# Performance work log

Measured on AMD Instinct MI355X. Metric: run time of the kernel, lower is better.

Reference implementation:

```python
import jax, jax.numpy as jnp
import numpy as np

B = 16384
D = 4096  # d_mlp == d_hidden in this module
K = 64


def setup_inputs() -> dict:
    key = jax.random.key(0)
    k1, k2, k3, k4 = jax.random.split(key, 4)
    x = jax.random.normal(k1, (B, D), dtype=jnp.float32)
    ema_frequency_counter = jax.random.uniform(k2, (D,), dtype=jnp.float32)
    W_enc = jax.random.normal(k3, (D, D), dtype=jnp.float32)
    # W_dec initialized like the module: randn, then scaled by 0.1/(norm+2*eps-ish);
    # the exact init scaling: norm over dim=1, norm += eps(=1), then *= 0.1/(norm+eps)
    W_dec_raw = jax.random.normal(k4, (D, D), dtype=jnp.float32)
    eps = 1.0
    norm = jnp.linalg.norm(W_dec_raw, axis=1, keepdims=True) + eps
    W_dec = W_dec_raw * (0.1 / (norm + eps))
    pre_bias = jnp.zeros((D,), dtype=jnp.float32)
    latent_bias = jnp.zeros((D,), dtype=jnp.float32)
    return {
        'x': x,
        'ema_frequency_counter': ema_frequency_counter,
        'W_enc': W_enc,
        'W_dec': W_dec,
        'pre_bias': pre_bias,
        'latent_bias': latent_bias,
        'k': K,
    }


def topk_activation(acts, k):
    # torch.topk -> ReLU on values -> scatter back into zeros
    vals, idx = jax.lax.top_k(acts, k)          # [B, k]
    vals = jax.nn.relu(vals)
    rows = jnp.arange(acts.shape[0])[:, None]   # [B, 1]
    return jnp.zeros_like(acts).at[rows, idx].set(vals)


def reference(x, ema_frequency_counter, W_enc, W_dec, pre_bias, latent_bias, k):
    # method='reconstruct' path of TopKAutoEncoder.forward
    x_center = x - pre_bias                     # [B, D]
    acts = x_center @ W_enc + latent_bias       # [B, D]
    acts_top_k = topk_activation(acts, k)       # sparse (k nonzeros/row)
    x_reconstruct = acts_top_k @ W_dec + pre_bias
    return x_reconstruct
```

## Files before the change

### kernel.cpp

```cpp
#include <hip/hip_runtime.h>
#include <hip/hip_bf16.h>
#include <stdint.h>


typedef _Float16 half8 __attribute__((ext_vector_type(8)));
typedef float f32x4 __attribute__((ext_vector_type(4)));
typedef unsigned short ushort8 __attribute__((ext_vector_type(8)));

#define B_ROWS 16384
#define D_DIM  4096
#define TOPK   64
#define MARGIN 0.25f
#define NTILES (D_DIM / 32)

__device__ __forceinline__ void gload_lds16(const void* g, void* l) {
  __builtin_amdgcn_global_load_lds(
      (const __attribute__((address_space(1))) unsigned int*)g,
      (__attribute__((address_space(3))) unsigned int*)l, 16, 0, 0);
}

__device__ __forceinline__ unsigned f32_sortable(float f) {
  unsigned u = __float_as_uint(f);
  return (u & 0x80000000u) ? ~u : (u | 0x80000000u);
}
__device__ __forceinline__ float sortable_f32(unsigned u) {
  return __uint_as_float((u & 0x80000000u) ? (u & 0x7fffffffu) : ~u);
}
__device__ __forceinline__ unsigned short f2bf(float f) {
  unsigned u = __float_as_uint(f);
  unsigned r = (u + 0x7fffu + ((u >> 16) & 1u)) >> 16;
  return (unsigned short)r;
}


__global__ __launch_bounds__(256) void conv_x(
    const float* __restrict__ x, const float* __restrict__ pre_bias,
    _Float16* __restrict__ Xh) {
  size_t g = ((size_t)blockIdx.x * 256 + threadIdx.x) * 8;
  int col = (int)(g & (D_DIM - 1));
  float4 a = *(const float4*)(x + g);
  float4 b = *(const float4*)(x + g + 4);
  float4 p = *(const float4*)(pre_bias + col);
  float4 q = *(const float4*)(pre_bias + col + 4);
  half8 h;
  h[0] = (_Float16)(a.x - p.x); h[1] = (_Float16)(a.y - p.y);
  h[2] = (_Float16)(a.z - p.z); h[3] = (_Float16)(a.w - p.w);
  h[4] = (_Float16)(b.x - q.x); h[5] = (_Float16)(b.y - q.y);
  h[6] = (_Float16)(b.z - q.z); h[7] = (_Float16)(b.w - q.w);
  *(half8*)(Xh + g) = h;
}

__global__ __launch_bounds__(256) void transp_w(
    const float* __restrict__ W, _Float16* __restrict__ WhT,
    float* __restrict__ WT) {
  __shared__ float tile[64][65];
  int bx = blockIdx.x, by = blockIdx.y;
  int tx = threadIdx.x & 63, ty4 = threadIdx.x >> 6;
  #pragma unroll 4
  for (int i = 0; i < 16; ++i) {
    int r = ty4 * 16 + i;
    tile[r][tx] = W[(size_t)(by * 64 + r) * D_DIM + bx * 64 + tx];
  }
  __syncthreads();
  #pragma unroll 4
  for (int i = 0; i < 16; ++i) {
    int r = ty4 * 16 + i;
    float v = tile[tx][r];
    size_t o = (size_t)(bx * 64 + r) * D_DIM + by * 64 + tx;
    WT[o] = v;
    WhT[o] = (_Float16)v;
  }
}

__global__ __launch_bounds__(256) void conv_wd(
    const float* __restrict__ W, unsigned short* __restrict__ o) {
  size_t g = ((size_t)blockIdx.x * 256 + threadIdx.x) * 8;
  float4 a = *(const float4*)(W + g);
  float4 b = *(const float4*)(W + g + 4);
  ushort8 v;
  v[0] = f2bf(a.x); v[1] = f2bf(a.y); v[2] = f2bf(a.z); v[3] = f2bf(a.w);
  v[4] = f2bf(b.x); v[5] = f2bf(b.y); v[6] = f2bf(b.z); v[7] = f2bf(b.w);
  *(ushort8*)(o + g) = v;
}


#define STAGE(T)                                                               \
  do {                                                                         \
    const int bo_ = ((T) & 3) * 8192;                                          \
    const int kk_ = (T) * 32;                                                  \
    gload_lds16(aSrc0 + kk_, AsB + bo_ + dst0);                                \
    gload_lds16(aSrc1 + kk_, AsB + bo_ + dst1);                                \
    gload_lds16(bSrc0 + kk_, BsB + bo_ + dst0);                                \
    gload_lds16(bSrc1 + kk_, BsB + bo_ + dst1);                                \
  } while (0)

#define PREFETCH(T, AF, BF)                                                    \
  do {                                                                         \
    const int ab_ = ((T) & 3) * 8192;                                          \
    _Pragma("unroll") for (int nj = 0; nj < 4; ++nj)                           \
        BF[nj] = *(const half8*)(BsB + ab_ + bBase + nj * 512);                \
    _Pragma("unroll") for (int mi = 0; mi < 4; ++mi)                           \
        AF[mi] = *(const half8*)(AsB + ab_ + aBase + mi * 512);                \
  } while (0)

#define BODY(T, AFC, BFC, AFN, BFN, VMSTR)                                     \
  do {                                                                         \
    asm volatile("s_waitcnt " VMSTR ::: "memory");                             \
    __builtin_amdgcn_s_barrier();                                              \
    asm volatile("" ::: "memory");                                             \
    if ((T) + 3 < NTILES) STAGE((T) + 3);                                      \
    if ((T) + 1 < NTILES) PREFETCH((T) + 1, AFN, BFN);                         \
    __builtin_amdgcn_s_setprio(1);                                             \
    _Pragma("unroll") for (int mi = 0; mi < 4; ++mi)                           \
        _Pragma("unroll") for (int nj = 0; nj < 4; ++nj)                       \
        acc[mi][nj] = __builtin_amdgcn_mfma_f32_16x16x32_f16(                  \
            AFC[mi], BFC[nj], acc[mi][nj], 0, 0, 0);                           \
    __builtin_amdgcn_s_setprio(0);                                             \
    {                                                                          \
      const int ab_ = ((T) & 3) * 8192;                                        \
      half8 af2[4];                                                            \
      _Pragma("unroll") for (int mi = 0; mi < 4; ++mi)                         \
          af2[mi] = *(const half8*)(AsB + ab_ + aBase + (mi + 4) * 512);       \
      __builtin_amdgcn_s_setprio(1);                                           \
      _Pragma("unroll") for (int mi = 0; mi < 4; ++mi)                         \
          _Pragma("unroll") for (int nj = 0; nj < 4; ++nj)                     \
          acc[mi + 4][nj] = __builtin_amdgcn_mfma_f32_16x16x32_f16(            \
              af2[mi], BFC[nj], acc[mi + 4][nj], 0, 0, 0);                     \
      __builtin_amdgcn_s_setprio(0);                                           \
    }                                                                          \
  } while (0)

__global__ __launch_bounds__(512, 2) void gemm_f16(
    const _Float16* __restrict__ A, const _Float16* __restrict__ Bt,
    const float* __restrict__ latent_bias, float* __restrict__ C) {
  extern __shared__ _Float16 ldsbuf[];
  _Float16* AsB = ldsbuf;
  _Float16* BsB = ldsbuf + 4 * 8192;

  const int tid = threadIdx.x;
  const int lane = tid & 63, wave = tid >> 6;
  const int wr = wave >> 2, wc = wave & 3;

  int bid = blockIdx.x;
  int swz = (bid & 7) * (1024 >> 3) + (bid >> 3);
  const int bmBase = (swz >> 4) * 256;
  const int bnBase = (swz & 15) * 256;

  const int i0 = tid, i1 = 512 + tid;
  const int s0 = i0 ^ ((i0 >> 3) & 3), s1 = i1 ^ ((i1 >> 3) & 3);
  const _Float16* aSrc0 = A + (size_t)(bmBase + (s0 >> 2)) * D_DIM + (s0 & 3) * 8;
  const _Float16* aSrc1 = A + (size_t)(bmBase + (s1 >> 2)) * D_DIM + (s1 & 3) * 8;
  const _Float16* bSrc0 = Bt + (size_t)(bnBase + (s0 >> 2)) * D_DIM + (s0 & 3) * 8;
  const _Float16* bSrc1 = Bt + (size_t)(bnBase + (s1 >> 2)) * D_DIM + (s1 & 3) * 8;
  const int dst0 = i0 * 8, dst1 = i1 * 8;

  const int fr = lane & 15, c4 = lane >> 4;
  const int swzc = (c4 ^ ((fr >> 1) & 3)) * 8;
  const int aBase = (wr * 128 + fr) * 32 + swzc;
  const int bBase = (wc * 64 + fr) * 32 + swzc;

  f32x4 acc[8][4];
  #pragma unroll
  for (int i = 0; i < 8; ++i)
    #pragma unroll
    for (int j = 0; j < 4; ++j) acc[i][j] = f32x4{0.f, 0.f, 0.f, 0.f};

  STAGE(0); STAGE(1); STAGE(2);
  asm volatile("s_waitcnt vmcnt(8)" ::: "memory");
  __builtin_amdgcn_s_barrier();
  asm volatile("" ::: "memory");
  half8 afA[4], bfA[4], afB[4], bfB[4];
  PREFETCH(0, afA, bfA);

  for (int t = 0; t < NTILES - 2; t += 2) {
    BODY(t, afA, bfA, afB, bfB, "vmcnt(4)");
    BODY(t + 1, afB, bfB, afA, bfA, "vmcnt(4)");
  }
  BODY(NTILES - 2, afA, bfA, afB, bfB, "vmcnt(0)");
  BODY(NTILES - 1, afB, bfB, afA, bfA, "vmcnt(0)");

  const int crow0 = bmBase + wr * 128 + c4 * 4;
  const int ccol0 = bnBase + wc * 64 + fr;
  #pragma unroll
  for (int mi = 0; mi < 8; ++mi)
    #pragma unroll
    for (int nj = 0; nj < 4; ++nj) {
      int col = ccol0 + nj * 16;
      float lb = latent_bias[col];
      #pragma unroll
      for (int r = 0; r < 4; ++r)
        C[(size_t)(crow0 + mi * 16 + r) * D_DIM + col] = acc[mi][nj][r] + lb;
    }
}


__global__ __launch_bounds__(256) void topk_classify(
    const float* __restrict__ acts, float* __restrict__ vals,
    int* __restrict__ idxs, int* __restrict__ ambIdx,
    int* __restrict__ rowMeta) {
  const int row = blockIdx.x;
  const int tid = threadIdx.x;
  const int lane = tid & 63, wave = tid >> 6;
  __shared__ int sred[4];
  const float* arow = acts + (size_t)row * D_DIM;
  unsigned su[16];
  #pragma unroll
  for (int i = 0; i < 4; ++i) {
    float4 a = *(const float4*)(arow + i * 1024 + tid * 4);
    su[4 * i + 0] = f32_sortable(a.x);
    su[4 * i + 1] = f32_sortable(a.y);
    su[4 * i + 2] = f32_sortable(a.z);
    su[4 * i + 3] = f32_sortable(a.w);
  }
  unsigned thr = 0u;
  for (int b = 31; b >= 12; --b) {
    unsigned cand = thr | (1u << b);
    int c = 0;
    #pragma unroll
    for (int i = 0; i < 16; ++i) c += (su[i] >= cand) ? 1 : 0;
    #pragma unroll
    for (int off = 32; off; off >>= 1) c += __shfl_down(c, off);
    if (lane == 0) sred[wave] = c;
    __syncthreads();
    int tot = sred[0] + sred[1] + sred[2] + sred[3];
    if (tot >= TOPK) thr = cand;
    __syncthreads();
  }
  float Tlo = sortable_f32(thr);
  float Thi = sortable_f32(thr + 4096u);
  unsigned uhi = f32_sortable(Thi + MARGIN);
  unsigned ulo = f32_sortable(Tlo - MARGIN);
  int mC = 0, aC = 0;
  #pragma unroll
  for (int i = 0; i < 16; ++i) {
    unsigned u = su[i];
    if (u > uhi) ++mC;
    else if (u >= ulo) ++aC;
  }
  int xs = mC | (aC << 16);
  #pragma unroll
  for (int off = 1; off < 64; off <<= 1) {
    int y = __shfl_up(xs, off);
    if (lane >= off) xs += y;
  }
  if (lane == 63) sred[wave] = xs;
  __syncthreads();
  int base = 0;
  for (int w = 0; w < 4; ++w)
    if (w < wave) base += sred[w];
  int tot = sred[0] + sred[1] + sred[2] + sred[3];
  int incl = base + xs;
  int mp = (incl & 0xffff) - mC;
  int ap = (incl >> 16) - aC;
  int mTot = tot & 0xffff, aTot = tot >> 16;
  const int need = TOPK - mTot;
  const bool fast = (aTot == need);
  #pragma unroll
  for (int e = 0; e < 16; ++e) {
    unsigned u = su[e];
    int d = (e >> 2) * 1024 + tid * 4 + (e & 3);
    if (u > uhi) {
      vals[(size_t)row * TOPK + mp] = fmaxf(sortable_f32(u), 0.0f);
      idxs[(size_t)row * TOPK + mp] = d;
      ++mp;
    } else if (u >= ulo) {
      if (fast) {
        vals[(size_t)row * TOPK + mTot + ap] = fmaxf(sortable_f32(u), 0.0f);
        idxs[(size_t)row * TOPK + mTot + ap] = d;
      } else if (ap < 128) {
        ambIdx[(size_t)row * 128 + ap] = d;
      }
      ++ap;
    }
  }
  if (tid == 0) {
    rowMeta[row * 2 + 0] = mTot;
    rowMeta[row * 2 + 1] = (fast || need <= 0) ? 0 : ((aTot > 128) ? 128 : aTot);
  }
}


__global__ __launch_bounds__(256) void rescue(
    const float* __restrict__ x, const float* __restrict__ WT,
    const float* __restrict__ pre_bias, const float* __restrict__ latent_bias,
    const float* __restrict__ acts, const int* __restrict__ ambIdx,
    const int* __restrict__ rowMeta, float* __restrict__ vals,
    int* __restrict__ idxs) {
  const int row = blockIdx.x;
  const int m = rowMeta[row * 2 + 0];
  const int s = rowMeta[row * 2 + 1];
  const int need = TOPK - m;
  const int tid = threadIdx.x;
  if (need <= 0 || s <= 0) return;
  if (s == need) {
    if (tid < s) {
      int d = ambIdx[(size_t)row * 128 + tid];
      float v = acts[(size_t)row * D_DIM + d];
      vals[(size_t)row * TOPK + m + tid] = fmaxf(v, 0.0f);
      idxs[(size_t)row * TOPK + m + tid] = d;
    }
    return;
  }
  __shared__ double exv[128];
  const int lane = tid & 63, wave = tid >> 6;
  const float* xr = x + (size_t)row * D_DIM;
  for (int c = wave; c < s; c += 4) {
    int d = ambIdx[(size_t)row * 128 + c];
    const float* wrow = WT + (size_t)d * D_DIM;
    double acc = 0.0;
    #pragma unroll 4
    for (int t = 0; t < 16; ++t) {
      int k0 = t * 256 + lane * 4;
      float4 xv = *(const float4*)(xr + k0);
      float4 pv = *(const float4*)(pre_bias + k0);
      float4 wv = *(const float4*)(wrow + k0);
      acc = fma((double)xv.x - (double)pv.x, (double)wv.x, acc);
      acc = fma((double)xv.y - (double)pv.y, (double)wv.y, acc);
      acc = fma((double)xv.z - (double)pv.z, (double)wv.z, acc);
      acc = fma((double)xv.w - (double)pv.w, (double)wv.w, acc);
    }
    #pragma unroll
    for (int off = 32; off; off >>= 1) acc += __shfl_down(acc, off);
    if (lane == 0) exv[c] = acc + (double)latent_bias[d];
  }
  __syncthreads();
  if (tid == 0) {
    for (int t = 0; t < need; ++t) {
      double best = -1.0e300; int besti = 1 << 30; int bestc = -1;
      for (int c = 0; c < s; ++c) {
        double v = exv[c];
        int d = ambIdx[(size_t)row * 128 + c];
        if (v > best || (v == best && d < besti)) {
          best = v; besti = d; bestc = c;
        }
      }
      vals[(size_t)row * TOPK + m + t] = fmaxf((float)best, 0.0f);
      idxs[(size_t)row * TOPK + m + t] = besti;
      exv[bestc] = -1.0e300;
    }
  }
}


__global__ __launch_bounds__(256) void reconstruct(
    const unsigned short* __restrict__ Wd, const float* __restrict__ vals,
    const int* __restrict__ idxs, const float* __restrict__ pre_bias,
    float* __restrict__ out) {
  const int bid = blockIdx.x;
  const int cb = bid & 7, rowblk = bid >> 3;
  const int tid = threadIdx.x, lane = tid & 63, wave = tid >> 6;
  const int row = rowblk * 4 + wave;
  const int col0 = cb * 512 + lane * 8;
  __shared__ float sval[256];
  __shared__ int sidx[256];
  sval[tid] = vals[(size_t)(rowblk * 4 + (tid >> 6)) * TOPK + (tid & 63)];
  sidx[tid] = idxs[(size_t)(rowblk * 4 + (tid >> 6)) * TOPK + (tid & 63)];
  __syncthreads();
  float acc[8];
  float4 p0 = *(const float4*)(pre_bias + col0);
  float4 p1 = *(const float4*)(pre_bias + col0 + 4);
  acc[0] = p0.x; acc[1] = p0.y; acc[2] = p0.z; acc[3] = p0.w;
  acc[4] = p1.x; acc[5] = p1.y; acc[6] = p1.z; acc[7] = p1.w;
  #pragma unroll 4
  for (int k = 0; k < TOPK; ++k) {
    float v = sval[wave * 64 + k];
    int d = sidx[wave * 64 + k];
    ushort8 w = *(const ushort8*)(Wd + (size_t)d * D_DIM + col0);
    #pragma unroll
    for (int j = 0; j < 8; ++j)
      acc[j] = fmaf(v, __uint_as_float(((unsigned)w[j]) << 16), acc[j]);
  }
  float4 o0 = {acc[0], acc[1], acc[2], acc[3]};
  float4 o1 = {acc[4], acc[5], acc[6], acc[7]};
  *(float4*)(out + (size_t)row * D_DIM + col0) = o0;
  *(float4*)(out + (size_t)row * D_DIM + col0 + 4) = o1;
}


extern "C" void kernel_launch(void* const* d_in, const int* in_sizes, int n_in,
                              void* d_out, int out_size, void* d_ws,
                              size_t ws_size, hipStream_t stream) {
  const float* x           = (const float*)d_in[0];
  const float* W_enc       = (const float*)d_in[2];
  const float* W_dec       = (const float*)d_in[3];
  const float* pre_bias    = (const float*)d_in[4];
  const float* latent_bias = (const float*)d_in[5];
  float* out = (float*)d_out;
  char* ws = (char*)d_ws;
  size_t off = 0;
  auto alloc = [&](size_t bytes) {
    size_t o = off;
    off = (off + bytes + 255) & ~(size_t)255;
    return o;
  };
  _Float16* Xh        = (_Float16*)(ws + alloc((size_t)B_ROWS * D_DIM * 2));
  _Float16* WhT       = (_Float16*)(ws + alloc((size_t)D_DIM * D_DIM * 2));
  float* WT           = (float*)(ws + alloc((size_t)D_DIM * D_DIM * 4));
  unsigned short* Wd  = (unsigned short*)(ws + alloc((size_t)D_DIM * D_DIM * 2));
  float* vals         = (float*)(ws + alloc((size_t)B_ROWS * TOPK * 4));
  int* idxs           = (int*)(ws + alloc((size_t)B_ROWS * TOPK * 4));
  int* ambIdx         = (int*)(ws + alloc((size_t)B_ROWS * 128 * 4));
  int* rowMeta        = (int*)(ws + alloc((size_t)B_ROWS * 2 * 4));
  (void)ws_size; (void)in_sizes; (void)n_in; (void)out_size;

  (void)hipFuncSetAttribute((const void*)gemm_f16,
                            hipFuncAttributeMaxDynamicSharedMemorySize,
                            131072);

  conv_x<<<(B_ROWS * D_DIM / 8) / 256, 256, 0, stream>>>(x, pre_bias, Xh);
  transp_w<<<dim3(D_DIM / 64, D_DIM / 64), 256, 0, stream>>>(W_enc, WhT, WT);
  conv_wd<<<((size_t)D_DIM * D_DIM / 8) / 256, 256, 0, stream>>>(W_dec, Wd);
  gemm_f16<<<(B_ROWS / 256) * (D_DIM / 256), 512, 131072, stream>>>(
      Xh, WhT, latent_bias, out);
  topk_classify<<<B_ROWS, 256, 0, stream>>>(out, vals, idxs, ambIdx, rowMeta);
  rescue<<<B_ROWS, 256, 0, stream>>>(x, WT, pre_bias, latent_bias, out,
                                     ambIdx, rowMeta, vals, idxs);
  reconstruct<<<(B_ROWS / 4) * 8, 256, 0, stream>>>(Wd, vals, idxs, pre_bias,
                                                    out);
}
```

Measured before the change: 1.209 ms.

## Rework encoder GEMM to 256x128 tiles with 32x32x16 MFMA and 3-stage LDS ring

The fp16 encoder GEMM now uses 256x128 block tiles instead of 256x256 and computes with 32x32x16 MFMA instructions. Each wave holds four 32x32 accumulators, where before it held a grid of 16x16 fragments. LDS drops to 72KB in a three-buffer ring so four blocks can share a CU, which aims to raise occupancy and latency hiding. In exchange, data reuse per block is lower and B traffic rises, and the register-level prefetch of fragments across iterations is gone.

```diff
diff --git a/kernel.cpp b/kernel.cpp
--- a/kernel.cpp
+++ b/kernel.cpp
@@ -5,6 +5,7 @@
 
 typedef _Float16 half8 __attribute__((ext_vector_type(8)));
 typedef float f32x4 __attribute__((ext_vector_type(4)));
+typedef float f32x16 __attribute__((ext_vector_type(16)));
 typedef unsigned short ushort8 __attribute__((ext_vector_type(8)));
 
 #define B_ROWS 16384
@@ -84,113 +85,100 @@
 }
 
 
-#define STAGE(T)                                                               \
+#define STAGE3(KK, BS)                                                         \
   do {                                                                         \
-    const int bo_ = ((T) & 3) * 8192;                                          \
-    const int kk_ = (T) * 32;                                                  \
-    gload_lds16(aSrc0 + kk_, AsB + bo_ + dst0);                                \
-    gload_lds16(aSrc1 + kk_, AsB + bo_ + dst1);                                \
-    gload_lds16(bSrc0 + kk_, BsB + bo_ + dst0);                                \
-    gload_lds16(bSrc1 + kk_, BsB + bo_ + dst1);                                \
+    gload_lds16(aSrc0 + (KK), lds + (BS) + dA0);                               \
+    gload_lds16(aSrc1 + (KK), lds + (BS) + dA1);                               \
+    gload_lds16(bSrc + (KK), lds + (BS) + dB);                                 \
   } while (0)
 
-#define PREFETCH(T, AF, BF)                                                    \
+#define GBODY(DOSTAGE, KK, VMSTR)                                              \
   do {                                                                         \
-    const int ab_ = ((T) & 3) * 8192;                                          \
-    _Pragma("unroll") for (int nj = 0; nj < 4; ++nj)                           \
-        BF[nj] = *(const half8*)(BsB + ab_ + bBase + nj * 512);                \
-    _Pragma("unroll") for (int mi = 0; mi < 4; ++mi)                           \
-        AF[mi] = *(const half8*)(AsB + ab_ + aBase + mi * 512);                \
-  } while (0)
-
-#define BODY(T, AFC, BFC, AFN, BFN, VMSTR)                                     \
-  do {                                                                         \
+    if (DOSTAGE) STAGE3((KK), boffS);                                          \
+    _Pragma("unroll") for (int ks = 0; ks < 2; ++ks) {                         \
+      const int kx = ks * 16;                       \
+      half8 a0 = *(const half8*)(lds + boffC + (aOff ^ kx));                   \
+      half8 a1 = *(const half8*)(lds + boffC + (aOff ^ kx) + 1024);            \
+      half8 b0 = *(const half8*)(lds + boffC + (bOff ^ kx));                   \
+      half8 b1 = *(const half8*)(lds + boffC + (bOff ^ kx) + 1024);            \
+      __builtin_amdgcn_s_setprio(1);                                           \
+      acc00 = __builtin_amdgcn_mfma_f32_32x32x16_f16(a0, b0, acc00, 0, 0, 0);  \
+      acc01 = __builtin_amdgcn_mfma_f32_32x32x16_f16(a0, b1, acc01, 0, 0, 0);  \
+      acc10 = __builtin_amdgcn_mfma_f32_32x32x16_f16(a1, b0, acc10, 0, 0, 0);  \
+      acc11 = __builtin_amdgcn_mfma_f32_32x32x16_f16(a1, b1, acc11, 0, 0, 0);  \
+      __builtin_amdgcn_s_setprio(0);                                           \
+    }                                                                          \
     asm volatile("s_waitcnt " VMSTR ::: "memory");                             \
     __builtin_amdgcn_s_barrier();                                              \
     asm volatile("" ::: "memory");                                             \
-    if ((T) + 3 < NTILES) STAGE((T) + 3);                                      \
-    if ((T) + 1 < NTILES) PREFETCH((T) + 1, AFN, BFN);                         \
-    __builtin_amdgcn_s_setprio(1);                                             \
-    _Pragma("unroll") for (int mi = 0; mi < 4; ++mi)                           \
-        _Pragma("unroll") for (int nj = 0; nj < 4; ++nj)                       \
-        acc[mi][nj] = __builtin_amdgcn_mfma_f32_16x16x32_f16(                  \
-            AFC[mi], BFC[nj], acc[mi][nj], 0, 0, 0);                           \
-    __builtin_amdgcn_s_setprio(0);                                             \
-    {                                                                          \
-      const int ab_ = ((T) & 3) * 8192;                                        \
-      half8 af2[4];                                                            \
-      _Pragma("unroll") for (int mi = 0; mi < 4; ++mi)                         \
-          af2[mi] = *(const half8*)(AsB + ab_ + aBase + (mi + 4) * 512);       \
-      __builtin_amdgcn_s_setprio(1);                                           \
-      _Pragma("unroll") for (int mi = 0; mi < 4; ++mi)                         \
-          _Pragma("unroll") for (int nj = 0; nj < 4; ++nj)                     \
-          acc[mi + 4][nj] = __builtin_amdgcn_mfma_f32_16x16x32_f16(            \
-              af2[mi], BFC[nj], acc[mi + 4][nj], 0, 0, 0);                     \
-      __builtin_amdgcn_s_setprio(0);                                           \
-    }                                                                          \
   } while (0)
 
-__global__ __launch_bounds__(512, 2) void gemm_f16(
+#define GROT()                                                                 \
+  do {                                                                         \
+    boffC += 12288; if (boffC == 36864) boffC = 0;                             \
+    boffS += 12288; if (boffS == 36864) boffS = 0;                             \
+  } while (0)
+
+__global__ __launch_bounds__(512, 4) void gemm_f16(
     const _Float16* __restrict__ A, const _Float16* __restrict__ Bt,
     const float* __restrict__ latent_bias, float* __restrict__ C) {
-  extern __shared__ _Float16 ldsbuf[];
-  _Float16* AsB = ldsbuf;
-  _Float16* BsB = ldsbuf + 4 * 8192;
-
+  extern __shared__ _Float16 lds[];
   const int tid = threadIdx.x;
-  const int lane = tid & 63, wave = tid >> 6;
-  const int wr = wave >> 2, wc = wave & 3;
+  const int lane = tid & 63, l31 = lane & 31, lhi = lane >> 5;
+  const int wave = tid >> 6, wvm = wave & 3, wvn = wave >> 2;
 
   int bid = blockIdx.x;
-  int swz = (bid & 7) * (1024 >> 3) + (bid >> 3);
-  const int bmBase = (swz >> 4) * 256;
-  const int bnBase = (swz & 15) * 256;
-
-  const int i0 = tid, i1 = 512 + tid;
-  const int s0 = i0 ^ ((i0 >> 3) & 3), s1 = i1 ^ ((i1 >> 3) & 3);
-  const _Float16* aSrc0 = A + (size_t)(bmBase + (s0 >> 2)) * D_DIM + (s0 & 3) * 8;
-  const _Float16* aSrc1 = A + (size_t)(bmBase + (s1 >> 2)) * D_DIM + (s1 & 3) * 8;
-  const _Float16* bSrc0 = Bt + (size_t)(bnBase + (s0 >> 2)) * D_DIM + (s0 & 3) * 8;
-  const _Float16* bSrc1 = Bt + (size_t)(bnBase + (s1 >> 2)) * D_DIM + (s1 & 3) * 8;
-  const int dst0 = i0 * 8, dst1 = i1 * 8;
-
-  const int fr = lane & 15, c4 = lane >> 4;
-  const int swzc = (c4 ^ ((fr >> 1) & 3)) * 8;
-  const int aBase = (wr * 128 + fr) * 32 + swzc;
-  const int bBase = (wc * 64 + fr) * 32 + swzc;
-
-  f32x4 acc[8][4];
-  #pragma unroll
-  for (int i = 0; i < 8; ++i)
-    #pragma unroll
-    for (int j = 0; j < 4; ++j) acc[i][j] = f32x4{0.f, 0.f, 0.f, 0.f};
-
-  STAGE(0); STAGE(1); STAGE(2);
-  asm volatile("s_waitcnt vmcnt(8)" ::: "memory");
+  int swz = (bid & 7) * (2048 >> 3) + (bid >> 3);
+  const int bmBase = (swz >> 5) * 256;
+  const int bnBase = (swz & 31) * 128;
+
+  const int pA0 = tid, pA1 = 512 + tid, pB = tid;
+  const int sA0 = pA0 ^ ((pA0 >> 3) & 3), sA1 = pA1 ^ ((pA1 >> 3) & 3);
+  const int sB = pB ^ ((pB >> 3) & 3);
+  const _Float16* aSrc0 = A + (size_t)(bmBase + (sA0 >> 2)) * D_DIM + (sA0 & 3) * 8;
+  const _Float16* aSrc1 = A + (size_t)(bmBase + (sA1 >> 2)) * D_DIM + (sA1 & 3) * 8;
+  const _Float16* bSrc  = Bt + (size_t)(bnBase + (sB >> 2)) * D_DIM + (sB & 3) * 8;
+  const int dA0 = pA0 * 8, dA1 = pA1 * 8, dB = 8192 + pB * 8;
+
+  const int cp0 = lhi ^ ((l31 >> 1) & 3);
+  const int aOff = (wvm * 64 + l31) * 32 + cp0 * 8;
+  const int bOff = 8192 + (wvn * 64 + l31) * 32 + cp0 * 8;
+
+  f32x16 acc00, acc01, acc10, acc11;
+  #pragma unroll
+  for (int i = 0; i < 16; ++i) {
+    acc00[i] = 0.f; acc01[i] = 0.f; acc10[i] = 0.f; acc11[i] = 0.f;
+  }
+
+  int boffC = 0, boffS = 24576;
+  STAGE3(0, 0);
+  STAGE3(32, 12288);
+  asm volatile("s_waitcnt vmcnt(3)" ::: "memory");
   __builtin_amdgcn_s_barrier();
   asm volatile("" ::: "memory");
-  half8 afA[4], bfA[4], afB[4], bfB[4];
-  PREFETCH(0, afA, bfA);
-
-  for (int t = 0; t < NTILES - 2; t += 2) {
-    BODY(t, afA, bfA, afB, bfB, "vmcnt(4)");
-    BODY(t + 1, afB, bfB, afA, bfA, "vmcnt(4)");
-  }
-  BODY(NTILES - 2, afA, bfA, afB, bfB, "vmcnt(0)");
-  BODY(NTILES - 1, afB, bfB, afA, bfA, "vmcnt(0)");
-
-  const int crow0 = bmBase + wr * 128 + c4 * 4;
-  const int ccol0 = bnBase + wc * 64 + fr;
-  #pragma unroll
-  for (int mi = 0; mi < 8; ++mi)
-    #pragma unroll
-    for (int nj = 0; nj < 4; ++nj) {
-      int col = ccol0 + nj * 16;
-      float lb = latent_bias[col];
-      #pragma unroll
-      for (int r = 0; r < 4; ++r)
-        C[(size_t)(crow0 + mi * 16 + r) * D_DIM + col] = acc[mi][nj][r] + lb;
-    }
+
+  for (int t = 0; t < NTILES - 3; ++t) {
+    GBODY(true, (t + 2) * 32, "vmcnt(3)");
+    GROT();
+  }
+  GBODY(true, (NTILES - 1) * 32, "vmcnt(0)");
+  GROT();
+  GBODY(false, 0, "vmcnt(0)");
+  GROT();
+  GBODY(false, 0, "vmcnt(0)");
+
+  const int crow0 = bmBase + wvm * 64;
+  const int ccol0 = bnBase + wvn * 64;
+  const float lb0 = latent_bias[ccol0 + l31];
+  const float lb1 = latent_bias[ccol0 + 32 + l31];
+  #pragma unroll
+  for (int r = 0; r < 16; ++r) {
+    const int rr = (r & 3) + 8 * (r >> 2) + 4 * lhi;
+    C[(size_t)(crow0 + rr) * D_DIM + ccol0 + l31] = acc00[r] + lb0;
+    C[(size_t)(crow0 + rr) * D_DIM + ccol0 + 32 + l31] = acc01[r] + lb1;
+    C[(size_t)(crow0 + 32 + rr) * D_DIM + ccol0 + l31] = acc10[r] + lb0;
+    C[(size_t)(crow0 + 32 + rr) * D_DIM + ccol0 + 32 + l31] = acc11[r] + lb1;
+  }
 }
 
 
@@ -405,12 +393,12 @@
 
   (void)hipFuncSetAttribute((const void*)gemm_f16,
                             hipFuncAttributeMaxDynamicSharedMemorySize,
-                            131072);
+                            73728);
 
   conv_x<<<(B_ROWS * D_DIM / 8) / 256, 256, 0, stream>>>(x, pre_bias, Xh);
   transp_w<<<dim3(D_DIM / 64, D_DIM / 64), 256, 0, stream>>>(W_enc, WhT, WT);
   conv_wd<<<((size_t)D_DIM * D_DIM / 8) / 256, 256, 0, stream>>>(W_dec, Wd);
-  gemm_f16<<<(B_ROWS / 256) * (D_DIM / 256), 512, 131072, stream>>>(
+  gemm_f16<<<(B_ROWS / 256) * (D_DIM / 128), 512, 73728, stream>>>(
       Xh, WhT, latent_bias, out);
   topk_classify<<<B_ROWS, 256, 0, stream>>>(out, vals, idxs, ambIdx, rowMeta);
   rescue<<<B_ROWS, 256, 0, stream>>>(x, WT, pre_bias, latent_bias, out,
```

New measurement: 1.321 ms. 9.3% more time.

## Restructure GEMM main loop into 8-wave ping-pong phases with 64-wide K tiles

Applied to the files above, without the earlier changes.

Replaces the 4-stage, 32-wide-K circular LDS pipeline with a double-buffered 64-wide-K scheme. Each K tile is split into four phases, each doing an LDS fragment read, one async global-to-LDS stage of A or B for the next tile, a barrier, and 16 MFMAs. The goal is to interleave memory staging with MFMA work more finely, in an hipBLASLt-style ping-pong schedule. It adds more barriers per tile and less prefetch depth, which could stall waves if global latency is not covered.

```diff
diff --git a/kernel.cpp b/kernel.cpp
--- a/kernel.cpp
+++ b/kernel.cpp
@@ -11,7 +11,7 @@
 #define D_DIM  4096
 #define TOPK   64
 #define MARGIN 0.25f
-#define NTILES (D_DIM / 32)
+#define KTILES (D_DIM / 64)
 
 __device__ __forceinline__ void gload_lds16(const void* g, void* l) {
   __builtin_amdgcn_global_load_lds(
@@ -84,59 +84,54 @@
 }
 
 
-#define STAGE(T)                                                               \
+#define STG_A(T, KH)                                                           \
   do {                                                                         \
-    const int bo_ = ((T) & 3) * 8192;                                          \
-    const int kk_ = (T) * 32;                                                  \
-    gload_lds16(aSrc0 + kk_, AsB + bo_ + dst0);                                \
-    gload_lds16(aSrc1 + kk_, AsB + bo_ + dst1);                                \
-    gload_lds16(bSrc0 + kk_, BsB + bo_ + dst0);                                \
-    gload_lds16(bSrc1 + kk_, BsB + bo_ + dst1);                                \
+    const int ds_ = ((T) & 1) * 32768 + (KH) * 8192;                           \
+    const int ko_ = (T) * 64 + (KH) * 32;                                      \
+    gload_lds16(aS0 + ko_, lds + ds_ + i0 * 8);                                \
+    gload_lds16(aS1 + ko_, lds + ds_ + i1 * 8);                                \
   } while (0)
 
-#define PREFETCH(T, AF, BF)                                                    \
+#define STG_B(T, KH)                                                           \
   do {                                                                         \
-    const int ab_ = ((T) & 3) * 8192;                                          \
-    _Pragma("unroll") for (int nj = 0; nj < 4; ++nj)                           \
-        BF[nj] = *(const half8*)(BsB + ab_ + bBase + nj * 512);                \
-    _Pragma("unroll") for (int mi = 0; mi < 4; ++mi)                           \
-        AF[mi] = *(const half8*)(AsB + ab_ + aBase + mi * 512);                \
+    const int ds_ = ((T) & 1) * 32768 + 16384 + (KH) * 8192;                   \
+    const int ko_ = (T) * 64 + (KH) * 32;                                      \
+    gload_lds16(bS0 + ko_, lds + ds_ + i0 * 8);                                \
+    gload_lds16(bS1 + ko_, lds + ds_ + i1 * 8);                                \
   } while (0)
 
-#define BODY(T, AFC, BFC, AFN, BFN, VMSTR)                                     \
+#define VMW(N) asm volatile("s_waitcnt vmcnt(" #N ")" ::: "memory")
+#define BARR()                                                                 \
   do {                                                                         \
-    asm volatile("s_waitcnt " VMSTR ::: "memory");                             \
+    asm volatile("" ::: "memory");                                             \
     __builtin_amdgcn_s_barrier();                                              \
     asm volatile("" ::: "memory");                                             \
-    if ((T) + 3 < NTILES) STAGE((T) + 3);                                      \
-    if ((T) + 1 < NTILES) PREFETCH((T) + 1, AFN, BFN);                         \
+  } while (0)
+
+#define PH(T, KK, MB, LOADB, STAGEOP)                                          \
+  do {                                                                         \
+    const int dC_ = ((T) & 1) * 32768 + (KK) * 8192;                           \
+    half8 af_[4];                                                              \
+    _Pragma("unroll") for (int mi = 0; mi < 4; ++mi)                           \
+        af_[mi] = *(const half8*)(lds + dC_ + aBase + ((MB) + mi) * 512);      \
+    if (LOADB) {                                                               \
+      _Pragma("unroll") for (int nj = 0; nj < 4; ++nj)                         \
+          bfr[nj] = *(const half8*)(lds + dC_ + 16384 + bBase + nj * 512);     \
+    }                                                                          \
+    STAGEOP;                                                                   \
+    BARR();                                                                    \
     __builtin_amdgcn_s_setprio(1);                                             \
     _Pragma("unroll") for (int mi = 0; mi < 4; ++mi)                           \
         _Pragma("unroll") for (int nj = 0; nj < 4; ++nj)                       \
-        acc[mi][nj] = __builtin_amdgcn_mfma_f32_16x16x32_f16(                  \
-            AFC[mi], BFC[nj], acc[mi][nj], 0, 0, 0);                           \
+        acc[(MB) + mi][nj] = __builtin_amdgcn_mfma_f32_16x16x32_f16(           \
+            af_[mi], bfr[nj], acc[(MB) + mi][nj], 0, 0, 0);                    \
     __builtin_amdgcn_s_setprio(0);                                             \
-    {                                                                          \
-      const int ab_ = ((T) & 3) * 8192;                                        \
-      half8 af2[4];                                                            \
-      _Pragma("unroll") for (int mi = 0; mi < 4; ++mi)                         \
-          af2[mi] = *(const half8*)(AsB + ab_ + aBase + (mi + 4) * 512);       \
-      __builtin_amdgcn_s_setprio(1);                                           \
-      _Pragma("unroll") for (int mi = 0; mi < 4; ++mi)                         \
-          _Pragma("unroll") for (int nj = 0; nj < 4; ++nj)                     \
-          acc[mi + 4][nj] = __builtin_amdgcn_mfma_f32_16x16x32_f16(            \
-              af2[mi], BFC[nj], acc[mi + 4][nj], 0, 0, 0);                     \
-      __builtin_amdgcn_s_setprio(0);                                           \
-    }                                                                          \
   } while (0)
 
 __global__ __launch_bounds__(512, 2) void gemm_f16(
     const _Float16* __restrict__ A, const _Float16* __restrict__ Bt,
     const float* __restrict__ latent_bias, float* __restrict__ C) {
-  extern __shared__ _Float16 ldsbuf[];
-  _Float16* AsB = ldsbuf;
-  _Float16* BsB = ldsbuf + 4 * 8192;
-
+  extern __shared__ _Float16 lds[];
   const int tid = threadIdx.x;
   const int lane = tid & 63, wave = tid >> 6;
   const int wr = wave >> 2, wc = wave & 3;
@@ -148,11 +143,10 @@
 
   const int i0 = tid, i1 = 512 + tid;
   const int s0 = i0 ^ ((i0 >> 3) & 3), s1 = i1 ^ ((i1 >> 3) & 3);
-  const _Float16* aSrc0 = A + (size_t)(bmBase + (s0 >> 2)) * D_DIM + (s0 & 3) * 8;
-  const _Float16* aSrc1 = A + (size_t)(bmBase + (s1 >> 2)) * D_DIM + (s1 & 3) * 8;
-  const _Float16* bSrc0 = Bt + (size_t)(bnBase + (s0 >> 2)) * D_DIM + (s0 & 3) * 8;
-  const _Float16* bSrc1 = Bt + (size_t)(bnBase + (s1 >> 2)) * D_DIM + (s1 & 3) * 8;
-  const int dst0 = i0 * 8, dst1 = i1 * 8;
+  const _Float16* aS0 = A + (size_t)(bmBase + (s0 >> 2)) * D_DIM + (s0 & 3) * 8;
+  const _Float16* aS1 = A + (size_t)(bmBase + (s1 >> 2)) * D_DIM + (s1 & 3) * 8;
+  const _Float16* bS0 = Bt + (size_t)(bnBase + (s0 >> 2)) * D_DIM + (s0 & 3) * 8;
+  const _Float16* bS1 = Bt + (size_t)(bnBase + (s1 >> 2)) * D_DIM + (s1 & 3) * 8;
 
   const int fr = lane & 15, c4 = lane >> 4;
   const int swzc = (c4 ^ ((fr >> 1) & 3)) * 8;
@@ -164,20 +158,29 @@
   for (int i = 0; i < 8; ++i)
     #pragma unroll
     for (int j = 0; j < 4; ++j) acc[i][j] = f32x4{0.f, 0.f, 0.f, 0.f};
-
-  STAGE(0); STAGE(1); STAGE(2);
-  asm volatile("s_waitcnt vmcnt(8)" ::: "memory");
-  __builtin_amdgcn_s_barrier();
-  asm volatile("" ::: "memory");
-  half8 afA[4], bfA[4], afB[4], bfB[4];
-  PREFETCH(0, afA, bfA);
-
-  for (int t = 0; t < NTILES - 2; t += 2) {
-    BODY(t, afA, bfA, afB, bfB, "vmcnt(4)");
-    BODY(t + 1, afB, bfB, afA, bfA, "vmcnt(4)");
-  }
-  BODY(NTILES - 2, afA, bfA, afB, bfB, "vmcnt(0)");
-  BODY(NTILES - 1, afB, bfB, afA, bfA, "vmcnt(0)");
+  half8 bfr[4];
+
+  STG_A(0, 0); STG_B(0, 0); STG_A(0, 1); STG_B(0, 1);
+  VMW(4);
+  BARR();
+
+  for (int t = 0; t < KTILES - 1; ++t) {
+    PH(t, 0, 0, true,  STG_A(t + 1, 0));
+    BARR();
+    PH(t, 0, 4, false, STG_B(t + 1, 0));
+    VMW(4); BARR();
+    PH(t, 1, 0, true,  STG_A(t + 1, 1));
+    BARR();
+    PH(t, 1, 4, false, STG_B(t + 1, 1));
+    VMW(4); BARR();
+  }
+  PH(KTILES - 1, 0, 0, true,  (void)0);
+  BARR();
+  PH(KTILES - 1, 0, 4, false, (void)0);
+  VMW(0); BARR();
+  PH(KTILES - 1, 1, 0, true,  (void)0);
+  BARR();
+  PH(KTILES - 1, 1, 4, false, (void)0);
 
   const int crow0 = bmBase + wr * 128 + c4 * 4;
   const int ccol0 = bnBase + wc * 64 + fr;
```

After: 1.208 ms. About the same (-0.1%).
